# Kernel tuning notes

Hardware: AMD Instinct MI355X
Metric: run time of the kernel (lower is better)

## Reference

```python
import math
import jax, jax.numpy as jnp
import numpy as np

D_MODEL = 768
N_HEADS = 12


def setup_inputs() -> dict:
    key = jax.random.key(0)
    kx, kw, kb = jax.random.split(key, 3)
    x = jax.random.normal(kx, (2, 2048, D_MODEL), dtype=jnp.float32)
    # nn.Linear(D, 3D): weight [3D, D], bias [3D]; init ~ U(-1/sqrt(D), 1/sqrt(D))
    bound = 1.0 / math.sqrt(D_MODEL)
    W_kqv = jax.random.uniform(kw, (3 * D_MODEL, D_MODEL), dtype=jnp.float32, minval=-bound, maxval=bound)
    b_kqv = jax.random.uniform(kb, (3 * D_MODEL,), dtype=jnp.float32, minval=-bound, maxval=bound)
    return {"x": x, "W_kqv": W_kqv, "b_kqv": b_kqv}


def reference(x, W_kqv, b_kqv):
    N, C, D = x.shape
    H = N_HEADS
    hd = D // H
    z = jnp.einsum('ncd,ed->nce', x, W_kqv) + b_kqv  # [N, C, 3D]
    # order in source: k first, then q, then v
    k = z[:, :, :D].reshape(N, C, H, hd).transpose(0, 2, 1, 3)       # [N,H,C,hd]
    q = z[:, :, D:2 * D].reshape(N, C, H, hd).transpose(0, 2, 1, 3)
    v = z[:, :, 2 * D:].reshape(N, C, H, hd).transpose(0, 2, 1, 3)
    # NOTE: faithful to source: scale by sqrt(D) (full model dim), not sqrt(head_dim)
    scores = jnp.einsum('nhqd,nhkd->nhqk', q, k) / math.sqrt(D)
    causal = jnp.tril(jnp.ones((C, C), dtype=bool))
    scores = jnp.where(causal, scores, -jnp.inf)
    attn = jax.nn.softmax(scores, axis=-1)
    out = jnp.einsum('nhqk,nhkd->nhqd', attn, v)  # [N,H,C,hd]
    return out.transpose(0, 2, 1, 3).reshape(N, C, D)
```

## Files before the change

kernel.cpp:

```cpp
#include <hip/hip_runtime.h>
#include <stdint.h>

#define D_MODEL 768
#define E3      2304
#define NCTX    2048
#define NH      12
#define HD      64
#define MROWS   4096
#define NHTOT   24

typedef __attribute__((ext_vector_type(8))) short short8;
typedef __attribute__((ext_vector_type(4))) short bf16x4;
typedef __attribute__((ext_vector_type(4))) float f32x4;

typedef __attribute__((address_space(3))) uint32_t lds_u32;
typedef __attribute__((address_space(1))) uint32_t glob_u32;

__device__ __forceinline__ void async_copy16(const void* g, void* l) {
    __builtin_amdgcn_global_load_lds((const glob_u32*)(uintptr_t)g,
                                     (lds_u32*)(uint32_t)(uintptr_t)l, 16, 0, 0);
}

__device__ __forceinline__ unsigned short f2bf(float f) {
    uint32_t u = __builtin_bit_cast(uint32_t, f);
    u += 0x7fffu + ((u >> 16) & 1u);
    return (unsigned short)(u >> 16);
}

__device__ __forceinline__ float fast_exp2(float x) {
#if __has_builtin(__builtin_amdgcn_exp2f)
    return __builtin_amdgcn_exp2f(x);
#else
    return __expf(x * 0.6931471805599453f);
#endif
}

__device__ __forceinline__ f32x4 mfma16_bf16(bf16x4 a, bf16x4 b, f32x4 c) {
#if defined(__HIP_DEVICE_COMPILE__)
    return __builtin_amdgcn_mfma_f32_16x16x16bf16_1k(a, b, c, 0, 0, 0);
#else
    (void)a; (void)b;
    return c;
#endif
}

__global__ void cast_bf16_kernel(const float* __restrict__ in, unsigned short* __restrict__ out) {
    int i = blockIdx.x * blockDim.x + threadIdx.x;
    float4 v = ((const float4*)in)[i];
    ushort4 o;
    o.x = f2bf(v.x); o.y = f2bf(v.y); o.z = f2bf(v.z); o.w = f2bf(v.w);
    ((ushort4*)out)[i] = o;
}

__global__ __launch_bounds__(256) void qkv_gemm(const unsigned short* __restrict__ A,
                                                const unsigned short* __restrict__ B,
                                                const float* __restrict__ bias,
                                                unsigned short* __restrict__ Zq,
                                                unsigned short* __restrict__ Kb,
                                                unsigned short* __restrict__ Vb) {
    __shared__ __attribute__((aligned(16))) unsigned short sA[128 * 64];
    __shared__ __attribute__((aligned(16))) unsigned short sB[96 * 64];

    const int tid  = threadIdx.x;
    const int wave = tid >> 6;
    const int lane = tid & 63;
    const int quad = lane >> 4;
    const int l15  = lane & 15;
    const int wm   = (wave >> 1) * 64;
    const int wn   = (wave & 1) * 48;
    const int row0 = blockIdx.y * 128;
    const int col0 = blockIdx.x * 96;

    const int srow   = lane & 7;
    const int schunk = (lane >> 3) * 8;

    f32x4 acc[4][3] = {};

    for (int k0 = 0; k0 < D_MODEL; k0 += 64) {
        __syncthreads();
#pragma unroll
        for (int c = 0; c < 4; ++c) {
            const int reg = wave * 4 + c;
            async_copy16(A + (size_t)(row0 + reg * 8 + srow) * D_MODEL + k0 + schunk, &sA[reg * 512]);
        }
#pragma unroll
        for (int c = 0; c < 3; ++c) {
            const int reg = wave * 3 + c;
            async_copy16(B + (size_t)(col0 + reg * 8 + srow) * D_MODEL + k0 + schunk, &sB[reg * 512]);
        }
        __syncthreads();

#pragma unroll
        for (int ks = 0; ks < 2; ++ks) {
            const int qoff = (ks * 4 + quad) * 64 + (l15 & 7) * 8;
            short8 aF[4], bF[3];
#pragma unroll
            for (int i = 0; i < 4; ++i)
                aF[i] = *(const short8*)&sA[((wm >> 3) + i * 2 + (l15 >> 3)) * 512 + qoff];
#pragma unroll
            for (int j = 0; j < 3; ++j)
                bF[j] = *(const short8*)&sB[((wn >> 3) + j * 2 + (l15 >> 3)) * 512 + qoff];
#pragma unroll
            for (int i = 0; i < 4; ++i)
#pragma unroll
                for (int j = 0; j < 3; ++j)
                    acc[i][j] = __builtin_amdgcn_mfma_f32_16x16x32_bf16(aF[i], bF[j], acc[i][j], 0, 0, 0);
        }
    }

    if (col0 < D_MODEL) {
#pragma unroll
        for (int j = 0; j < 3; ++j) {
            const int col = col0 + wn + j * 16 + l15;
            const float bv = bias[col];
            const int h = col >> 6, d = col & 63;
            const int ks = d >> 5, quadd = (d >> 3) & 3, e = d & 7;
#pragma unroll
            for (int i = 0; i < 4; ++i) {
                const int row = row0 + wm + i * 16 + quad * 4;
                const int n = row >> 11;
                const int key = row & (NCTX - 1);
                const int kb = key >> 6;
                const int ct = (key >> 4) & 3;
                const size_t base = ((size_t)((n * NH + h) * 32 + kb)) * 4096
                                  + (((ks * 4 + ct) * 4 + quadd) * 16) * 8 + e;
#pragma unroll
                for (int r = 0; r < 4; ++r)
                    Kb[base + (size_t)(quad * 4 + r) * 8] = f2bf(acc[i][j][r] + bv);
            }
        }
    } else if (col0 < 2 * D_MODEL) {
        const float zscale = 0.036084391824351615f * 1.4426950408889634f;
#pragma unroll
        for (int j = 0; j < 3; ++j) {
            const int colz = col0 + wn + j * 16 + l15;
            const float bv = bias[colz];
            const int col = colz - D_MODEL;
#pragma unroll
            for (int i = 0; i < 4; ++i) {
                const int row = row0 + wm + i * 16 + quad * 4;
#pragma unroll
                for (int r = 0; r < 4; ++r)
                    Zq[(size_t)(row + r) * D_MODEL + col] = f2bf((acc[i][j][r] + bv) * zscale);
            }
        }
    } else {
#pragma unroll
        for (int j = 0; j < 3; ++j) {
            const int col = col0 + wn + j * 16 + l15;
            const float bv = bias[col];
            const int ch = col - 2 * D_MODEL;
            const int h = ch >> 6, d = ch & 63;
            const int dt = d >> 4, l15d = d & 15;
#pragma unroll
            for (int i = 0; i < 4; ++i) {
                const int row = row0 + wm + i * 16 + quad * 4;
                const int n = row >> 11;
                const int key = row & (NCTX - 1);
                const int kb = key >> 6;
                const int ct = (key >> 4) & 3;
                ushort4 w4;
                w4.x = f2bf(acc[i][j][0] + bv);
                w4.y = f2bf(acc[i][j][1] + bv);
                w4.z = f2bf(acc[i][j][2] + bv);
                w4.w = f2bf(acc[i][j][3] + bv);
                *(ushort4*)&Vb[((size_t)((n * NH + h) * 32 + kb)) * 4096
                               + (((ct * 4 + dt) * 4 + quad) * 16 + l15d) * 4] = w4;
            }
        }
    }
}

__global__ __launch_bounds__(256) void attn_kernel(const unsigned short* __restrict__ Zq,
                                                   const unsigned short* __restrict__ Kb,
                                                   const unsigned short* __restrict__ Vb,
                                                   float* __restrict__ out) {
    __shared__ __attribute__((aligned(16))) unsigned short sK[2][4096];

    const int tid  = threadIdx.x;
    const int wave = tid >> 6;
    const int lane = tid & 63;
    const int quad = lane >> 4;
    const int l15  = lane & 15;
    const int b    = blockIdx.x;
    const int nh   = (b & 7) * 3 + ((b >> 3) % 3);
    const int t    = (NCTX / 64 - 1) - b / NHTOT;
    const int n    = nh / NH;
    const int h    = nh - n * NH;

    const unsigned short* KbP = Kb + (size_t)(nh * 32) * 4096;
    const unsigned short* VbP = Vb + (size_t)(nh * 32) * 4096;

    const unsigned short* Qp = Zq + (size_t)(n * NCTX + t * 64 + wave * 16) * D_MODEL + h * HD;
    short8 qf[2];
#pragma unroll
    for (int ks = 0; ks < 2; ++ks)
        qf[ks] = *(const short8*)&Qp[(size_t)l15 * D_MODEL + ks * 32 + quad * 8];

    f32x4 o[4] = {};
    float lsum = 0.0f;

#pragma unroll
    for (int c = 0; c < 2; ++c) {
        const int off = wave * 1024 + c * 512;
        async_copy16(KbP + off + lane * 8, &sK[0][off]);
    }

    for (int kb = 0; kb <= t; ++kb) {
        const int buf = kb & 1;
        __syncthreads();
        if (kb < t) {
#pragma unroll
            for (int c = 0; c < 2; ++c) {
                const int off = wave * 1024 + c * 512;
                async_copy16(KbP + (size_t)(kb + 1) * 4096 + off + lane * 8, &sK[buf ^ 1][off]);
            }
        }

        bf16x4 vf[4][4];
#pragma unroll
        for (int ct = 0; ct < 4; ++ct)
#pragma unroll
            for (int dt = 0; dt < 4; ++dt)
                vf[ct][dt] = *(const bf16x4*)&VbP[(size_t)kb * 4096 + (ct * 4 + dt) * 256 + lane * 4];

        short8 kf[2][4];
#pragma unroll
        for (int ks = 0; ks < 2; ++ks)
#pragma unroll
            for (int ct = 0; ct < 4; ++ct)
                kf[ks][ct] = *(const short8*)&sK[buf][(ks * 4 + ct) * 512 + lane * 8];

        f32x4 s[4] = {};
#pragma unroll
        for (int ct = 0; ct < 4; ++ct) {
            s[ct] = __builtin_amdgcn_mfma_f32_16x16x32_bf16(kf[0][ct], qf[0], s[ct], 0, 0, 0);
            s[ct] = __builtin_amdgcn_mfma_f32_16x16x32_bf16(kf[1][ct], qf[1], s[ct], 0, 0, 0);
        }

        const bool diag = (kb == t);
        const int qg = t * 64 + wave * 16 + l15;
        bf16x4 pA[4];
#pragma unroll
        for (int ct = 0; ct < 4; ++ct) {
            float pv[4];
#pragma unroll
            for (int r = 0; r < 4; ++r) {
                const int key = kb * 64 + ct * 16 + quad * 4 + r;
                float sv = s[ct][r];
                if (diag && key > qg) sv = -INFINITY;
                pv[r] = fast_exp2(sv);
                lsum += pv[r];
            }
            pA[ct][0] = (short)f2bf(pv[0]); pA[ct][1] = (short)f2bf(pv[1]);
            pA[ct][2] = (short)f2bf(pv[2]); pA[ct][3] = (short)f2bf(pv[3]);
        }

#pragma unroll
        for (int ct = 0; ct < 4; ++ct)
#pragma unroll
            for (int dt = 0; dt < 4; ++dt)
                o[dt] = mfma16_bf16(pA[ct], vf[ct][dt], o[dt]);
    }

    float l = lsum;
    l += __shfl_xor(l, 16);
    l += __shfl_xor(l, 32);
    const float linv = 1.0f / l;
#pragma unroll
    for (int r = 0; r < 4; ++r) {
        const float inv = __shfl(linv, quad * 4 + r);
        const size_t row = (size_t)n * NCTX + t * 64 + wave * 16 + quad * 4 + r;
#pragma unroll
        for (int dt = 0; dt < 4; ++dt)
            out[row * D_MODEL + h * HD + dt * 16 + l15] = o[dt][r] * inv;
    }
}

extern "C" void kernel_launch(void* const* d_in, const int* in_sizes, int n_in,
                              void* d_out, int out_size, void* d_ws, size_t ws_size,
                              hipStream_t stream) {
    const float* x = (const float*)d_in[0];
    const float* W = (const float*)d_in[1];
    const float* b = (const float*)d_in[2];
    float* out = (float*)d_out;

    unsigned short* xb = (unsigned short*)d_ws;
    unsigned short* Wb = xb + (size_t)MROWS * D_MODEL;
    unsigned short* Zq = Wb + (size_t)E3 * D_MODEL;
    unsigned short* Kb = Zq + (size_t)MROWS * D_MODEL;
    unsigned short* Vb = Kb + (size_t)NHTOT * 32 * 4096;

    cast_bf16_kernel<<<dim3((MROWS * D_MODEL / 4) / 256), 256, 0, stream>>>(x, xb);
    cast_bf16_kernel<<<dim3((E3 * D_MODEL / 4) / 256), 256, 0, stream>>>(W, Wb);
    qkv_gemm<<<dim3(E3 / 96, MROWS / 128), 256, 0, stream>>>(xb, Wb, b, Zq, Kb, Vb);
    attn_kernel<<<dim3(NHTOT * (NCTX / 64)), 256, 0, stream>>>(Zq, Kb, Vb, out);
}
```

Baseline: 155.6 us.

## Register-prefetch GEMM tiles and stage V through double-buffered LDS in attention

The QKV GEMM replaces the async global-to-LDS copies with register prefetch of the next k-tile, overlapped with MFMA on the current one. Fragments are read from LDS before a barrier, and the prefetched data is stored after the MFMAs. The attention kernel now double-buffers V tiles in LDS via async copies instead of loading V fragments straight from global memory each iteration, and the head mapping changes to a simple modulo. This aims to hide global load latency in both kernels, at the cost of more LDS use and more registers.

New measurement: 148.5 us. 4.5% less time.

```diff
diff --git a/kernel.cpp b/kernel.cpp
--- a/kernel.cpp
+++ b/kernel.cpp
@@ -41,6 +41,15 @@
 #else
     (void)a; (void)b;
     return c;
+#endif
+}
+
+__device__ __forceinline__ void barrier_lgkm() {
+#if defined(__HIP_DEVICE_COMPILE__)
+    asm volatile("" ::: "memory");
+    __builtin_amdgcn_s_waitcnt(0xC07F);
+    __builtin_amdgcn_s_barrier();
+    asm volatile("" ::: "memory");
 #endif
 }
 
@@ -74,37 +83,69 @@
     const int srow   = lane & 7;
     const int schunk = (lane >> 3) * 8;
 
+    const unsigned short* gA[4];
+    const unsigned short* gB[3];
+#pragma unroll
+    for (int c = 0; c < 4; ++c)
+        gA[c] = A + (size_t)(row0 + (wave * 4 + c) * 8 + srow) * D_MODEL + schunk;
+#pragma unroll
+    for (int c = 0; c < 3; ++c)
+        gB[c] = B + (size_t)(col0 + (wave * 3 + c) * 8 + srow) * D_MODEL + schunk;
+
+    unsigned short* const dA = &sA[(wave * 4) * 512 + lane * 8];
+    unsigned short* const dB = &sB[(wave * 3) * 512 + lane * 8];
+
+    short8 ra[4], rb[3];
+
+#pragma unroll
+    for (int c = 0; c < 4; ++c) ra[c] = *(const short8*)(gA[c]);
+#pragma unroll
+    for (int c = 0; c < 3; ++c) rb[c] = *(const short8*)(gB[c]);
+#pragma unroll
+    for (int c = 0; c < 4; ++c) *(short8*)(dA + c * 512) = ra[c];
+#pragma unroll
+    for (int c = 0; c < 3; ++c) *(short8*)(dB + c * 512) = rb[c];
+
     f32x4 acc[4][3] = {};
 
     for (int k0 = 0; k0 < D_MODEL; k0 += 64) {
-        __syncthreads();
-#pragma unroll
-        for (int c = 0; c < 4; ++c) {
-            const int reg = wave * 4 + c;
-            async_copy16(A + (size_t)(row0 + reg * 8 + srow) * D_MODEL + k0 + schunk, &sA[reg * 512]);
-        }
-#pragma unroll
-        for (int c = 0; c < 3; ++c) {
-            const int reg = wave * 3 + c;
-            async_copy16(B + (size_t)(col0 + reg * 8 + srow) * D_MODEL + k0 + schunk, &sB[reg * 512]);
-        }
-        __syncthreads();
-
+        barrier_lgkm();
+
+        const bool more = (k0 + 64 < D_MODEL);
+        if (more) {
+#pragma unroll
+            for (int c = 0; c < 4; ++c) ra[c] = *(const short8*)(gA[c] + k0 + 64);
+#pragma unroll
+            for (int c = 0; c < 3; ++c) rb[c] = *(const short8*)(gB[c] + k0 + 64);
+        }
+
+        short8 aF[2][4], bF[2][3];
 #pragma unroll
         for (int ks = 0; ks < 2; ++ks) {
             const int qoff = (ks * 4 + quad) * 64 + (l15 & 7) * 8;
-            short8 aF[4], bF[3];
 #pragma unroll
             for (int i = 0; i < 4; ++i)
-                aF[i] = *(const short8*)&sA[((wm >> 3) + i * 2 + (l15 >> 3)) * 512 + qoff];
+                aF[ks][i] = *(const short8*)&sA[((wm >> 3) + i * 2 + (l15 >> 3)) * 512 + qoff];
 #pragma unroll
             for (int j = 0; j < 3; ++j)
-                bF[j] = *(const short8*)&sB[((wn >> 3) + j * 2 + (l15 >> 3)) * 512 + qoff];
+                bF[ks][j] = *(const short8*)&sB[((wn >> 3) + j * 2 + (l15 >> 3)) * 512 + qoff];
+        }
+
+        barrier_lgkm();
+
+#pragma unroll
+        for (int ks = 0; ks < 2; ++ks)
 #pragma unroll
             for (int i = 0; i < 4; ++i)
 #pragma unroll
                 for (int j = 0; j < 3; ++j)
-                    acc[i][j] = __builtin_amdgcn_mfma_f32_16x16x32_bf16(aF[i], bF[j], acc[i][j], 0, 0, 0);
+                    acc[i][j] = __builtin_amdgcn_mfma_f32_16x16x32_bf16(aF[ks][i], bF[ks][j], acc[i][j], 0, 0, 0);
+
+        if (more) {
+#pragma unroll
+            for (int c = 0; c < 4; ++c) *(short8*)(dA + c * 512) = ra[c];
+#pragma unroll
+            for (int c = 0; c < 3; ++c) *(short8*)(dB + c * 512) = rb[c];
         }
     }
 
@@ -176,6 +217,7 @@
                                                    const unsigned short* __restrict__ Vb,
                                                    float* __restrict__ out) {
     __shared__ __attribute__((aligned(16))) unsigned short sK[2][4096];
+    __shared__ __attribute__((aligned(16))) unsigned short sV[2][4096];
 
     const int tid  = threadIdx.x;
     const int wave = tid >> 6;
@@ -183,7 +225,7 @@
     const int quad = lane >> 4;
     const int l15  = lane & 15;
     const int b    = blockIdx.x;
-    const int nh   = (b & 7) * 3 + ((b >> 3) % 3);
+    const int nh   = b % NHTOT;
     const int t    = (NCTX / 64 - 1) - b / NHTOT;
     const int n    = nh / NH;
     const int h    = nh - n * NH;
@@ -204,6 +246,7 @@
     for (int c = 0; c < 2; ++c) {
         const int off = wave * 1024 + c * 512;
         async_copy16(KbP + off + lane * 8, &sK[0][off]);
+        async_copy16(VbP + off + lane * 8, &sV[0][off]);
     }
 
     for (int kb = 0; kb <= t; ++kb) {
@@ -214,15 +257,9 @@
             for (int c = 0; c < 2; ++c) {
                 const int off = wave * 1024 + c * 512;
                 async_copy16(KbP + (size_t)(kb + 1) * 4096 + off + lane * 8, &sK[buf ^ 1][off]);
-            }
-        }
-
-        bf16x4 vf[4][4];
-#pragma unroll
-        for (int ct = 0; ct < 4; ++ct)
-#pragma unroll
-            for (int dt = 0; dt < 4; ++dt)
-                vf[ct][dt] = *(const bf16x4*)&VbP[(size_t)kb * 4096 + (ct * 4 + dt) * 256 + lane * 4];
+                async_copy16(VbP + (size_t)(kb + 1) * 4096 + off + lane * 8, &sV[buf ^ 1][off]);
+            }
+        }
 
         short8 kf[2][4];
 #pragma unroll
@@ -259,8 +296,10 @@
 #pragma unroll
         for (int ct = 0; ct < 4; ++ct)
 #pragma unroll
-            for (int dt = 0; dt < 4; ++dt)
-                o[dt] = mfma16_bf16(pA[ct], vf[ct][dt], o[dt]);
+            for (int dt = 0; dt < 4; ++dt) {
+                const bf16x4 vf = *(const bf16x4*)&sV[buf][(ct * 4 + dt) * 256 + lane * 4];
+                o[dt] = mfma16_bf16(pA[ct], vf, o[dt]);
+            }
     }
 
     float l = lsum;
```
